# Kernel tuning notes

Measured on AMD Instinct MI355X. Metric: run time of the kernel, lower is better.

Reference implementation:

```python
import jax, jax.numpy as jnp
import numpy as np

L = 4        # num_layers
H = 1024     # hidden_size
NH = 16      # num_heads
KVH = 4      # num_kv_heads
QPK = NH // KVH
HD = H // NH # head_dim = 64
FF = 4096    # intermediate_size
V = 32000    # vocab_size
B, S = 2, 2048
EPS = 1e-5
STD = 0.02


def layernorm(x, g, b):
    m = jnp.mean(x, axis=-1, keepdims=True)
    v = jnp.mean(jnp.square(x - m), axis=-1, keepdims=True)
    return (x - m) * jax.lax.rsqrt(v + EPS) * g + b


def setup_inputs() -> dict:
    key = jax.random.key(0)
    ks = iter(jax.random.split(key, 24))
    n = lambda shape: STD * jax.random.normal(next(ks), shape, dtype=jnp.float32)
    KV = H * KVH // NH  # kv_size = 256
    inp = {
        'input_ids': jax.random.randint(next(ks), (B, S), 0, V),
        'attention_mask': jnp.zeros((B, S), dtype=jnp.float32),
        'tok_emb': n((V, H)),
        'pos_emb': n((S, H)),
        # per-layer stacked weights, stored [in, out] so y = x @ W + b
        'Wq': n((L, H, H)),  'bq': jnp.zeros((L, H)),
        'Wk': n((L, H, KV)), 'bk': jnp.zeros((L, KV)),
        'Wv': n((L, H, KV)), 'bv': jnp.zeros((L, KV)),
        'Wo': n((L, H, H)),  'bo': jnp.zeros((L, H)),
        'W1': n((L, H, FF)), 'b1': jnp.zeros((L, FF)),
        'W2': n((L, FF, H)), 'b2': jnp.zeros((L, H)),
        'ln1_g': jnp.ones((L, H)), 'ln1_b': jnp.zeros((L, H)),
        'ln2_g': jnp.ones((L, H)), 'ln2_b': jnp.zeros((L, H)),
        'lnf_g': jnp.ones((H,)),   'lnf_b': jnp.zeros((H,)),
        'Whead': n((H, V)),  # head has no bias
    }
    return inp


def gpt_forward(input_ids, attention_mask, tok_emb, pos_emb,
                Wq, bq, Wk, bk, Wv, bv, Wo, bo,
                W1, b1, W2, b2, ln1_g, ln1_b, ln2_g, ln2_b,
                lnf_g, lnf_b, Whead):
    b, s = input_ids.shape
    x = tok_emb[input_ids] + pos_emb[None, :s, :]  # [b,s,H]
    mask = attention_mask[:, None, None, None, :]  # [b,1,1,1,s] additive
    scale = 1.0 / jnp.sqrt(jnp.float32(HD))
    for l in range(L):
        h = layernorm(x, ln1_g[l], ln1_b[l])
        q = h @ Wq[l] + bq[l]                              # [b,s,H]
        k = h @ Wk[l] + bk[l]                              # [b,s,KV]
        v = h @ Wv[l] + bv[l]
        q = q.reshape(b, s, KVH, QPK, HD).transpose(0, 2, 3, 1, 4)  # [b,g,q,s,d]
        k = k.reshape(b, s, KVH, HD).transpose(0, 2, 1, 3)          # [b,g,s,d]
        v = v.reshape(b, s, KVH, HD).transpose(0, 2, 1, 3)
        scores = jnp.einsum('bgqsd,bgkd->bgqsk', q, k) * scale      # [b,g,q,s,s]
        scores = scores + mask
        w = jax.nn.softmax(scores, axis=-1)
        o = jnp.einsum('bgqsk,bgkd->bgqsd', w, v)                   # [b,g,q,s,d]
        o = o.transpose(0, 3, 1, 2, 4).reshape(b, s, H)
        x = x + (o @ Wo[l] + bo[l])
        h2 = layernorm(x, ln2_g[l], ln2_b[l])
        ff = jax.nn.gelu(h2 @ W1[l] + b1[l], approximate=False) @ W2[l] + b2[l]
        x = x + ff
    x = layernorm(x, lnf_g, lnf_b)
    return x @ Whead  # [b,s,V] logits


def reference(input_ids, attention_mask, tok_emb, pos_emb,
              Wq, bq, Wk, bk, Wv, bv, Wo, bo,
              W1, b1, W2, b2, ln1_g, ln1_b, ln2_g, ln2_b,
              lnf_g, lnf_b, Whead):
    return gpt_forward(input_ids, attention_mask, tok_emb, pos_emb,
                       Wq, bq, Wk, bk, Wv, bv, Wo, bo,
                       W1, b1, W2, b2, ln1_g, ln1_b, ln2_g, ln2_b,
                       lnf_g, lnf_b, Whead)
```

## Files before the change

### kernel.cpp

```cpp
#include <hip/hip_runtime.h>
#include <hip/hip_bf16.h>

#define LAYERS 4
#define H 1024
#define NH 16
#define KVH 4
#define HD 64
#define KVD 256
#define FF 4096
#define VOC 32000
#define BB 2
#define SS 2048
#define MROWS (BB*SS)
#define QKVN 1536

typedef __attribute__((ext_vector_type(4))) float f32x4;
typedef __attribute__((ext_vector_type(8))) short short8;
typedef __attribute__((ext_vector_type(4))) unsigned short u16x4;
typedef __attribute__((ext_vector_type(2))) unsigned int u32x2;

__device__ inline unsigned short f2bf(float f){
  union { float f; unsigned u; } v; v.f = f;
  return (unsigned short)((v.u + 0x7FFFu + ((v.u >> 16) & 1u)) >> 16);
}
__device__ inline unsigned cvt_pk_bf16(float a, float b){
  unsigned r;
  asm("v_cvt_pk_bf16_f32 %0, %1, %2" : "=v"(r) : "v"(a), "v"(b));
  return r;
}

__global__ __launch_bounds__(256) void embed_kernel(const int* __restrict__ ids,
    const float* __restrict__ tok, const float* __restrict__ pos, float* __restrict__ x)
{
  int row = blockIdx.x;
  int s = row & (SS-1);
  int id = ids[row];
  int t = threadIdx.x;
  f32x4 a = *(const f32x4*)&tok[(size_t)id*H + t*4];
  f32x4 p = *(const f32x4*)&pos[(size_t)s*H + t*4];
  *(f32x4*)&x[(size_t)row*H + t*4] = a + p;
}

__global__ __launch_bounds__(256) void ln_kernel(const float* __restrict__ x,
    const float* __restrict__ g, const float* __restrict__ b, unsigned short* __restrict__ out)
{
  int row = blockIdx.x;
  int t = threadIdx.x;
  const float* xr = x + (size_t)row*H;
  f32x4 v = *(const f32x4*)&xr[t*4];
  float s  = v[0]+v[1]+v[2]+v[3];
  float s2 = v[0]*v[0]+v[1]*v[1]+v[2]*v[2]+v[3]*v[3];
  #pragma unroll
  for (int off=1; off<64; off<<=1){ s += __shfl_xor(s,off); s2 += __shfl_xor(s2,off); }
  __shared__ float red[8];
  int w = t>>6;
  if ((t&63)==0){ red[w]=s; red[4+w]=s2; }
  __syncthreads();
  float S1 = red[0]+red[1]+red[2]+red[3];
  float S2 = red[4]+red[5]+red[6]+red[7];
  float mean = S1 * (1.0f/H);
  float var  = S2 * (1.0f/H) - mean*mean;
  float rs = rsqrtf(var + 1e-5f);
  u16x4 o;
  #pragma unroll
  for (int i=0;i<4;i++) o[i] = f2bf((v[i]-mean)*rs*g[t*4+i] + b[t*4+i]);
  *(u16x4*)&out[(size_t)row*H + t*4] = o;
}

__global__ __launch_bounds__(256) void convT_kernel(const float* __restrict__ in,
    unsigned short* __restrict__ out, int K, int N, size_t istride, size_t ostride)
{
  __shared__ float t[32][33];
  in  += (size_t)blockIdx.z * istride;
  out += (size_t)blockIdx.z * ostride;
  int n0 = blockIdx.x*32, k0 = blockIdx.y*32;
  int x = threadIdx.x & 31, y = threadIdx.x >> 5;
  #pragma unroll
  for (int j=0;j<4;j++) t[y+j*8][x] = in[(size_t)(k0+y+j*8)*N + n0 + x];
  __syncthreads();
  int x2 = threadIdx.x & 15, y2 = threadIdx.x >> 4;
  #pragma unroll
  for (int j=0;j<2;j++){
    int n = y2 + j*16;
    unsigned lo = f2bf(t[x2*2][n]);
    unsigned hi = f2bf(t[x2*2+1][n]);
    *(unsigned*)&out[(size_t)(n0+n)*K + k0 + x2*2] = lo | (hi<<16);
  }
}

__global__ __launch_bounds__(256) void bcat_kernel(const float* __restrict__ bq,
    const float* __restrict__ bk, const float* __restrict__ bv, float* __restrict__ out)
{
  int l = blockIdx.x, t = threadIdx.x;
  #pragma unroll
  for (int i=0;i<4;i++) out[l*QKVN + t + i*256] = bq[l*H + t + i*256];
  out[l*QKVN + 1024 + t] = bk[l*KVD + t];
  out[l*QKVN + 1280 + t] = bv[l*KVD + t];
}

template<int EPI>
__global__ __launch_bounds__(256) void gemm_bt(
    const unsigned short* __restrict__ A, const unsigned short* __restrict__ Bt,
    const float* __restrict__ bias, const float* __restrict__ res,
    float* __restrict__ outf, unsigned short* __restrict__ outb,
    unsigned short* __restrict__ outb2, unsigned short* __restrict__ outb3, int N, int K)
{
  __shared__ unsigned short As[128*32];
  __shared__ unsigned short Bs[128*32];
  int m0 = blockIdx.x*128, n0 = blockIdx.y*128;
  int tid = threadIdx.x;
  int lane = tid & 63, w = tid >> 6;
  int wr = (w>>1)*64, wc = (w&1)*64;
  int fr = lane & 15, fq = lane >> 4;
  f32x4 acc[4][4] = {};
  int srow = lane >> 2;
  int scol = (lane & 3) * 8;
  const unsigned short* a0 = A  + (size_t)m0*K + scol;
  const unsigned short* b0 = Bt + (size_t)n0*K + scol;
  for (int k0 = 0; k0 < K; k0 += 32){
    __syncthreads();
    #pragma unroll
    for (int c = 0; c < 2; c++){
      int ch = w*2 + c;
      int row = ch*16 + srow;
      __builtin_amdgcn_global_load_lds(
        (const __attribute__((address_space(1))) void*)(a0 + (size_t)row*K + k0),
        (__attribute__((address_space(3))) void*)(As + ch*512), 16, 0, 0);
      __builtin_amdgcn_global_load_lds(
        (const __attribute__((address_space(1))) void*)(b0 + (size_t)row*K + k0),
        (__attribute__((address_space(3))) void*)(Bs + ch*512), 16, 0, 0);
    }
    __syncthreads();
    short8 af[4], bf[4];
    #pragma unroll
    for (int mi=0;mi<4;mi++) af[mi] = *(const short8*)&As[(wr+mi*16+fr)*32 + fq*8];
    #pragma unroll
    for (int ni=0;ni<4;ni++) bf[ni] = *(const short8*)&Bs[(wc+ni*16+fr)*32 + fq*8];
    #pragma unroll
    for (int mi=0;mi<4;mi++)
      #pragma unroll
      for (int ni=0;ni<4;ni++)
        acc[mi][ni] = __builtin_amdgcn_mfma_f32_16x16x32_bf16(af[mi], bf[ni], acc[mi][ni], 0,0,0);
  }
  #pragma unroll
  for (int mi=0;mi<4;mi++)
    #pragma unroll
    for (int ni=0;ni<4;ni++){
      int col = n0 + wc + ni*16 + fr;
      float bi = (EPI==3) ? 0.0f : bias[col];
      #pragma unroll
      for (int r=0;r<4;r++){
        int row = m0 + wr + mi*16 + fq*4 + r;
        float vv = acc[mi][ni][r] + bi;
        if (EPI==1)      { size_t idx=(size_t)row*N+col; outf[idx] = vv + res[idx]; }
        else if (EPI==2) { size_t idx=(size_t)row*N+col; outb[idx] = f2bf(0.5f*vv*(1.0f+erff(vv*0.70710678118f))); }
        else if (EPI==3) { size_t idx=(size_t)row*N+col; outf[idx] = vv; }
        else if (EPI==5) {
          if (col < 1024)      outb [(size_t)row*H + col]            = f2bf(vv);
          else if (col < 1280) outb2[(size_t)row*KVD + (col-1024)]   = f2bf(vv);
          else                 outb3[(size_t)(col-1280)*MROWS + row] = f2bf(vv);
        }
      }
    }
}

template<int EPI>
__global__ __launch_bounds__(512, 2) void gemm256(
    const unsigned short* __restrict__ A, const unsigned short* __restrict__ Bt,
    const float* __restrict__ bias, float* __restrict__ outf,
    unsigned short* __restrict__ outb, int N, int K)
{
  __shared__ __align__(16) char lds[131072];
  const int tid = threadIdx.x;
  const int lane = tid & 63, wid = tid >> 6;
  const int wr = wid >> 2, wc = wid & 3;
  const int fr = lane & 15, fq = lane >> 4;
  const int m0 = blockIdx.x*256, n0 = blockIdx.y*256;
  const int nt = K >> 6;
  f32x4 acc[8][4] = {};

  #define STAGEH(PTR, baserow, kt, kk, ldsoff) do {                              \
    _Pragma("unroll")                                                            \
    for (int c=0;c<2;c++){                                                       \
      int r = c*128 + (tid>>2);                                                  \
      int ss = (tid&3) ^ ((r>>1)&3);                                             \
      __builtin_amdgcn_global_load_lds(                                          \
        (const __attribute__((address_space(1))) void*)((PTR) + (size_t)((baserow)+r)*K + (kt)*64 + (kk)*32 + ss*8), \
        (__attribute__((address_space(3))) void*)(lds + (ldsoff) + c*8192 + wid*1024), 16, 0, 0); \
    }                                                                            \
  } while(0)

  #define RD_A(buf,kk,row) (*(const short8*)(lds + ((buf)*2+(kk))*16384 + (row)*64 + ((fq ^ (((row)>>1)&3))*16)))
  #define RD_B(buf,kk,row) (*(const short8*)(lds + 65536 + ((buf)*2+(kk))*16384 + (row)*64 + ((fq ^ (((row)>>1)&3))*16)))

  STAGEH(A,  m0, 0, 0, 0);
  STAGEH(Bt, n0, 0, 0, 65536);
  STAGEH(A,  m0, 0, 1, 16384);
  STAGEH(Bt, n0, 0, 1, 65536+16384);
  asm volatile("s_waitcnt vmcnt(4)" ::: "memory");
  __builtin_amdgcn_s_barrier();

  for (int t = 0; t < nt; ++t){
    const int buf = t & 1, nb = buf ^ 1;
    const int kt1 = (t+1 < nt) ? t+1 : t;
    short8 bf[4], af[4];
    #pragma unroll
    for (int ni=0;ni<4;ni++) bf[ni] = RD_B(buf,0, wc*64+ni*16+fr);
    #pragma unroll
    for (int mi=0;mi<4;mi++) af[mi] = RD_A(buf,0, wr*128+mi*16+fr);
    STAGEH(A, m0, kt1, 0, (nb*2+0)*16384);
    __builtin_amdgcn_s_barrier();
    asm volatile("s_waitcnt lgkmcnt(0)" ::: "memory");
    __builtin_amdgcn_s_setprio(1);
    #pragma unroll
    for (int mi=0;mi<4;mi++)
      #pragma unroll
      for (int ni=0;ni<4;ni++)
        acc[mi][ni] = __builtin_amdgcn_mfma_f32_16x16x32_bf16(af[mi], bf[ni], acc[mi][ni], 0,0,0);
    __builtin_amdgcn_s_setprio(0);
    __builtin_amdgcn_s_barrier();
    #pragma unroll
    for (int mi=0;mi<4;mi++) af[mi] = RD_A(buf,0, wr*128+(4+mi)*16+fr);
    STAGEH(Bt, n0, kt1, 0, 65536+(nb*2+0)*16384);
    __builtin_amdgcn_s_barrier();
    asm volatile("s_waitcnt lgkmcnt(0)" ::: "memory");
    __builtin_amdgcn_s_setprio(1);
    #pragma unroll
    for (int mi=0;mi<4;mi++)
      #pragma unroll
      for (int ni=0;ni<4;ni++)
        acc[4+mi][ni] = __builtin_amdgcn_mfma_f32_16x16x32_bf16(af[mi], bf[ni], acc[4+mi][ni], 0,0,0);
    __builtin_amdgcn_s_setprio(0);
    asm volatile("s_waitcnt vmcnt(4)" ::: "memory");
    __builtin_amdgcn_s_barrier();
    #pragma unroll
    for (int ni=0;ni<4;ni++) bf[ni] = RD_B(buf,1, wc*64+ni*16+fr);
    #pragma unroll
    for (int mi=0;mi<4;mi++) af[mi] = RD_A(buf,1, wr*128+mi*16+fr);
    STAGEH(A, m0, kt1, 1, (nb*2+1)*16384);
    __builtin_amdgcn_s_barrier();
    asm volatile("s_waitcnt lgkmcnt(0)" ::: "memory");
    __builtin_amdgcn_s_setprio(1);
    #pragma unroll
    for (int mi=0;mi<4;mi++)
      #pragma unroll
      for (int ni=0;ni<4;ni++)
        acc[mi][ni] = __builtin_amdgcn_mfma_f32_16x16x32_bf16(af[mi], bf[ni], acc[mi][ni], 0,0,0);
    __builtin_amdgcn_s_setprio(0);
    __builtin_amdgcn_s_barrier();
    #pragma unroll
    for (int mi=0;mi<4;mi++) af[mi] = RD_A(buf,1, wr*128+(4+mi)*16+fr);
    STAGEH(Bt, n0, kt1, 1, 65536+(nb*2+1)*16384);
    __builtin_amdgcn_s_barrier();
    asm volatile("s_waitcnt lgkmcnt(0)" ::: "memory");
    __builtin_amdgcn_s_setprio(1);
    #pragma unroll
    for (int mi=0;mi<4;mi++)
      #pragma unroll
      for (int ni=0;ni<4;ni++)
        acc[4+mi][ni] = __builtin_amdgcn_mfma_f32_16x16x32_bf16(af[mi], bf[ni], acc[4+mi][ni], 0,0,0);
    __builtin_amdgcn_s_setprio(0);
    asm volatile("s_waitcnt vmcnt(4)" ::: "memory");
    __builtin_amdgcn_s_barrier();
  }
  #undef STAGEH
  #undef RD_A
  #undef RD_B

  #pragma unroll
  for (int mi=0; mi<8; mi++)
    #pragma unroll
    for (int ni=0; ni<4; ni++){
      int col = n0 + wc*64 + ni*16 + fr;
      float bi = (EPI==3) ? 0.0f : bias[col];
      #pragma unroll
      for (int r=0; r<4; r++){
        int row = m0 + wr*128 + mi*16 + fq*4 + r;
        float vv = acc[mi][ni][r] + bi;
        size_t idx = (size_t)row*N + col;
        if (EPI==3) outf[idx] = vv;
        else        outb[idx] = f2bf(0.5f*vv*(1.0f+erff(vv*0.70710678118f)));
      }
    }
}

#define LOG2E 1.4426950408889634f
__global__ __launch_bounds__(256) void attn_kernel(
    const unsigned short* __restrict__ q, const unsigned short* __restrict__ kptr,
    const unsigned short* __restrict__ vt, const float* __restrict__ mask,
    unsigned short* __restrict__ o)
{
  __shared__ char Pbuf[4][4096];
  int tid = threadIdx.x;
  int lane = tid & 63, wid = tid >> 6;
  int fr = lane & 15, fq = lane >> 4, fo = fq*8;
  int h = blockIdx.y, b = blockIdx.z, g = h >> 2;
  int qcol = h*HD, kcol = g*HD;
  int qbase = b*SS + blockIdx.x*128 + wid*32;
  char* Pl = Pbuf[wid];
  int swz = (fr & 7) << 4;

  short8 bq[2][2];
  #pragma unroll
  for (int h2=0; h2<2; h2++){
    const unsigned short* qrow = q + (size_t)(qbase + h2*16 + fr)*H + qcol;
    bq[h2][0] = *(const short8*)(qrow + fo);
    bq[h2][1] = *(const short8*)(qrow + 32 + fo);
  }

  f32x4 oacc[2][4] = {};
  float mrun[2] = {-1e30f, -1e30f}, lsum[2] = {0.f, 0.f};
  const float sc2 = 0.125f * LOG2E;

  const unsigned short* kp[4];
  #pragma unroll
  for (int f=0; f<4; f++) kp[f] = kptr + (size_t)(b*SS + f*16 + fr)*KVD + kcol + fo;
  const unsigned short* vp[4];
  #pragma unroll
  for (int dc=0; dc<4; dc++) vp[dc] = vt + (size_t)(kcol + dc*16 + fr)*MROWS + b*SS + fo;
  const float* mp = mask + b*SS + fq*4;

  short8 kaA[4][2], kaB[4][2];
  #pragma unroll
  for (int f=0; f<4; f++){
    kaA[f][0] = *(const short8*)(kp[f]);
    kaA[f][1] = *(const short8*)(kp[f] + 32);
    kp[f] += 64*KVD;
  }

#define ATTN_STEP(KA, KB, PF) do {                                             \
    f32x4 mkv[4];                                                              \
    _Pragma("unroll")                                                          \
    for (int f=0; f<4; f++) mkv[f] = *(const f32x4*)(mp + f*16);               \
    short8 va[4][2];                                                           \
    _Pragma("unroll")                                                          \
    for (int dc=0; dc<4; dc++){                                                \
      va[dc][0] = *(const short8*)(vp[dc]);                                    \
      va[dc][1] = *(const short8*)(vp[dc] + 32);                               \
    }                                                                          \
    f32x4 sf[2][4] = {};                                                       \
    __builtin_amdgcn_s_setprio(1);                                             \
    _Pragma("unroll")                                                          \
    for (int h2=0; h2<2; h2++)                                                 \
      _Pragma("unroll")                                                        \
      for (int f=0; f<4; f++){                                                 \
        sf[h2][f] = __builtin_amdgcn_mfma_f32_16x16x32_bf16(KA[f][0], bq[h2][0], sf[h2][f],0,0,0); \
        sf[h2][f] = __builtin_amdgcn_mfma_f32_16x16x32_bf16(KA[f][1], bq[h2][1], sf[h2][f],0,0,0); \
      }                                                                        \
    __builtin_amdgcn_s_setprio(0);                                             \
    if (PF){                                                                   \
      _Pragma("unroll")                                                        \
      for (int f=0; f<4; f++){                                                 \
        KB[f][0] = *(const short8*)(kp[f]);                                    \
        KB[f][1] = *(const short8*)(kp[f] + 32);                               \
        kp[f] += 64*KVD;                                                       \
      }                                                                        \
    }                                                                          \
    _Pragma("unroll")                                                          \
    for (int f=0; f<4; f++){                                                   \
      _Pragma("unroll")                                                        \
      for (int r=0; r<4; r++){                                                 \
        float m2 = mkv[f][r]*LOG2E;                                            \
        sf[0][f][r] = sf[0][f][r]*sc2 + m2;                                    \
        sf[1][f][r] = sf[1][f][r]*sc2 + m2;                                    \
      }                                                                        \
    }                                                                          \
    float pm[2];                                                               \
    _Pragma("unroll")                                                          \
    for (int h2=0; h2<2; h2++){                                                \
      float a0 = fmaxf(fmaxf(sf[h2][0][0],sf[h2][0][1]), fmaxf(sf[h2][0][2],sf[h2][0][3])); \
      float a1 = fmaxf(fmaxf(sf[h2][1][0],sf[h2][1][1]), fmaxf(sf[h2][1][2],sf[h2][1][3])); \
      float a2 = fmaxf(fmaxf(sf[h2][2][0],sf[h2][2][1]), fmaxf(sf[h2][2][2],sf[h2][2][3])); \
      float a3 = fmaxf(fmaxf(sf[h2][3][0],sf[h2][3][1]), fmaxf(sf[h2][3][2],sf[h2][3][3])); \
      float p = fmaxf(fmaxf(a0,a1), fmaxf(a2,a3));                             \
      p = fmaxf(p, __shfl_xor(p, 16));                                         \
      p = fmaxf(p, __shfl_xor(p, 32));                                         \
      pm[h2] = p;                                                              \
    }                                                                          \
    if (!__all(pm[0] <= mrun[0]+8.f && pm[1] <= mrun[1]+8.f)){                 \
      float al[2];                                                             \
      _Pragma("unroll")                                                        \
      for (int h2=0; h2<2; h2++){                                              \
        float mn = fmaxf(mrun[h2], pm[h2]);                                    \
        al[h2] = __builtin_amdgcn_exp2f(mrun[h2]-mn);                          \
        mrun[h2] = mn;                                                         \
        lsum[h2] *= al[h2];                                                    \
      }                                                                        \
      _Pragma("unroll")                                                        \
      for (int r=0; r<4; r++){                                                 \
        float altl = __shfl(al[0], fq*4+r);                                    \
        float alth = __shfl(al[1], fq*4+r);                                    \
        _Pragma("unroll")                                                      \
        for (int dc=0; dc<4; dc++){ oacc[0][dc][r]*=altl; oacc[1][dc][r]*=alth; } \
      }                                                                        \
    }                                                                          \
    _Pragma("unroll")                                                          \
    for (int h2=0; h2<2; h2++){                                                \
      float ps = 0.f;                                                          \
      _Pragma("unroll")                                                        \
      for (int f=0; f<4; f++)                                                  \
        _Pragma("unroll")                                                      \
        for (int r=0; r<4; r++){                                               \
          float e = __builtin_amdgcn_exp2f(sf[h2][f][r]-mrun[h2]);             \
          sf[h2][f][r] = e; ps += e;                                           \
        }                                                                      \
      ps += __shfl_xor(ps, 16);                                                \
      ps += __shfl_xor(ps, 32);                                                \
      lsum[h2] += ps;                                                          \
    }                                                                          \
    _Pragma("unroll")                                                          \
    for (int h2=0; h2<2; h2++){                                                \
      int prow = h2*16 + fr;                                                   \
      _Pragma("unroll")                                                        \
      for (int f=0; f<4; f++){                                                 \
        u32x2 pw;                                                              \
        pw[0] = cvt_pk_bf16(sf[h2][f][0], sf[h2][f][1]);                       \
        pw[1] = cvt_pk_bf16(sf[h2][f][2], sf[h2][f][3]);                       \
        *(u32x2*)(Pl + prow*128 + ((f*32 + fq*8) ^ swz)) = pw;                 \
      }                                                                        \
    }                                                                          \
    __builtin_amdgcn_s_setprio(1);                                             \
    _Pragma("unroll")                                                          \
    for (int h2=0; h2<2; h2++){                                                \
      int prow = h2*16 + fr;                                                   \
      _Pragma("unroll")                                                        \
      for (int gs=0; gs<2; gs++){                                              \
        short8 pa = *(const short8*)(Pl + prow*128 + ((gs*64 + fq*16) ^ swz)); \
        _Pragma("unroll")                                                      \
        for (int dc=0; dc<4; dc++)                                             \
          oacc[h2][dc] = __builtin_amdgcn_mfma_f32_16x16x32_bf16(pa, va[dc][gs], oacc[h2][dc],0,0,0); \
      }                                                                        \
    }                                                                          \
    __builtin_amdgcn_s_setprio(0);                                             \
    _Pragma("unroll")                                                          \
    for (int dc=0; dc<4; dc++) vp[dc] += 64;                                   \
    mp += 64;                                                                  \
  } while(0)

  for (int it = 0; it < SS/128 - 1; ++it){
    ATTN_STEP(kaA, kaB, 1);
    ATTN_STEP(kaB, kaA, 1);
  }
  ATTN_STEP(kaA, kaB, 1);
  ATTN_STEP(kaB, kaA, 0);
#undef ATTN_STEP

  #pragma unroll
  for (int h2=0; h2<2; h2++){
    float lt[4];
    #pragma unroll
    for (int r=0; r<4; r++) lt[r] = __shfl(lsum[h2], fq*4+r);
    #pragma unroll
    for (int dc=0; dc<4; dc++)
      #pragma unroll
      for (int r=0; r<4; r++){
        int row = qbase + h2*16 + fq*4 + r;
        o[(size_t)row*H + qcol + dc*16 + fr] = f2bf(oacc[h2][dc][r] / lt[r]);
      }
  }
}

extern "C" void kernel_launch(void* const* d_in, const int* in_sizes, int n_in,
                              void* d_out, int out_size, void* d_ws, size_t ws_size,
                              hipStream_t stream)
{
  const int*   ids  = (const int*)  d_in[0];
  const float* mask = (const float*)d_in[1];
  const float* tok  = (const float*)d_in[2];
  const float* pos  = (const float*)d_in[3];
  const float* Wq   = (const float*)d_in[4];
  const float* bq   = (const float*)d_in[5];
  const float* Wk   = (const float*)d_in[6];
  const float* bk   = (const float*)d_in[7];
  const float* Wv   = (const float*)d_in[8];
  const float* bv   = (const float*)d_in[9];
  const float* Wo   = (const float*)d_in[10];
  const float* bo   = (const float*)d_in[11];
  const float* W1   = (const float*)d_in[12];
  const float* b1   = (const float*)d_in[13];
  const float* W2   = (const float*)d_in[14];
  const float* b2   = (const float*)d_in[15];
  const float* ln1g = (const float*)d_in[16];
  const float* ln1b = (const float*)d_in[17];
  const float* ln2g = (const float*)d_in[18];
  const float* ln2b = (const float*)d_in[19];
  const float* lnfg = (const float*)d_in[20];
  const float* lnfb = (const float*)d_in[21];
  const float* Wh   = (const float*)d_in[22];
  float* out = (float*)d_out;

  char* ws = (char*)d_ws;
  float*          x    = (float*)ws;          ws += (size_t)MROWS*H*4;
  unsigned short* hb   = (unsigned short*)ws; ws += (size_t)MROWS*H*2;
  unsigned short* qb   = (unsigned short*)ws; ws += (size_t)MROWS*H*2;
  unsigned short* kb   = (unsigned short*)ws; ws += (size_t)MROWS*KVD*2;
  unsigned short* vtb  = (unsigned short*)ws; ws += (size_t)KVD*MROWS*2;
  unsigned short* ob   = (unsigned short*)ws; ws += (size_t)MROWS*H*2;
  unsigned short* f1   = (unsigned short*)ws; ws += (size_t)MROWS*FF*2;
  unsigned short* Wqkv = (unsigned short*)ws; ws += (size_t)LAYERS*QKVN*H*2;
  unsigned short* WoT  = (unsigned short*)ws; ws += (size_t)LAYERS*H*H*2;
  unsigned short* W1T  = (unsigned short*)ws; ws += (size_t)LAYERS*H*FF*2;
  unsigned short* W2T  = (unsigned short*)ws; ws += (size_t)LAYERS*H*FF*2;
  unsigned short* WhT  = (unsigned short*)ws; ws += (size_t)H*VOC*2;
  float*          bcat = (float*)ws;          ws += (size_t)LAYERS*QKVN*4;

  convT_kernel<<<dim3(H/32,   H/32,  LAYERS), 256, 0, stream>>>(Wq, Wqkv,          H,  H,   (size_t)H*H,   (size_t)QKVN*H);
  convT_kernel<<<dim3(KVD/32, H/32,  LAYERS), 256, 0, stream>>>(Wk, Wqkv + 1024*H, H,  KVD, (size_t)H*KVD, (size_t)QKVN*H);
  convT_kernel<<<dim3(KVD/32, H/32,  LAYERS), 256, 0, stream>>>(Wv, Wqkv + 1280*H, H,  KVD, (size_t)H*KVD, (size_t)QKVN*H);
  convT_kernel<<<dim3(H/32,   H/32,  LAYERS), 256, 0, stream>>>(Wo, WoT,           H,  H,   (size_t)H*H,   (size_t)H*H);
  convT_kernel<<<dim3(FF/32,  H/32,  LAYERS), 256, 0, stream>>>(W1, W1T,           H,  FF,  (size_t)H*FF,  (size_t)H*FF);
  convT_kernel<<<dim3(H/32,   FF/32, LAYERS), 256, 0, stream>>>(W2, W2T,           FF, H,   (size_t)FF*H,  (size_t)FF*H);
  convT_kernel<<<dim3(VOC/32, H/32,  1),      256, 0, stream>>>(Wh, WhT,           H,  VOC, 0, 0);
  bcat_kernel<<<LAYERS, 256, 0, stream>>>(bq, bk, bv, bcat);

  embed_kernel<<<MROWS, 256, 0, stream>>>(ids, tok, pos, x);
  for (int l=0; l<LAYERS; l++){
    ln_kernel<<<MROWS,256,0,stream>>>(x, ln1g + l*H, ln1b + l*H, hb);
    gemm_bt<5><<<dim3(MROWS/128, QKVN/128),256,0,stream>>>(hb, Wqkv + (size_t)l*QKVN*H, bcat + l*QKVN, nullptr, nullptr, qb, kb, vtb, QKVN, H);
    attn_kernel<<<dim3(SS/128, NH, BB), 256, 0, stream>>>(qb, kb, vtb, mask, ob);
    gemm_bt<1><<<dim3(MROWS/128, H/128),  256,0,stream>>>(ob, WoT + (size_t)l*H*H,  bo + l*H,  x, x, nullptr, nullptr, nullptr, H, H);
    ln_kernel<<<MROWS,256,0,stream>>>(x, ln2g + l*H, ln2b + l*H, hb);
    gemm256<2><<<dim3(MROWS/256, FF/256), 512,0,stream>>>(hb, W1T + (size_t)l*H*FF, b1 + l*FF, nullptr, f1, FF, H);
    gemm_bt<1><<<dim3(MROWS/128, H/128),  256,0,stream>>>(f1, W2T + (size_t)l*H*FF, b2 + l*H,  x, x, nullptr, nullptr, nullptr, H, FF);
  }
  ln_kernel<<<MROWS,256,0,stream>>>(x, lnfg, lnfb, hb);
  gemm256<3><<<dim3(MROWS/256, VOC/256), 512,0,stream>>>(hb, WhT, nullptr, out, nullptr, VOC, H);
}
```

Measured before the change: 1.989 ms.

## Deepen GEMM pipelines to 4-stage LDS ring and remap workgroups across XCDs

The small 128x128 GEMM moves from a single-buffered, fully synchronised loop to a 4-stage global_load_lds ring with swizzled LDS, prefetching three k-tiles ahead and waiting with vmcnt, so loads overlap MFMA work. The 256x256 GEMM switches from a 2-buffer scheme with 64-wide k-tiles to a 4-buffer ring with 32-wide k-tiles. It also remaps block IDs so each XCD gets a contiguous range of tiles, which should improve L2 reuse. The cost is more LDS per block in gemm_bt, which may limit occupancy, plus added launch-bounds pressure on registers.

Result: faster. 1.688 ms (-15.2%).

```diff
diff --git a/kernel.cpp b/kernel.cpp
--- a/kernel.cpp
+++ b/kernel.cpp
@@ -99,49 +99,67 @@
 }
 
 template<int EPI>
-__global__ __launch_bounds__(256) void gemm_bt(
+__global__ __launch_bounds__(256, 2) void gemm_bt(
     const unsigned short* __restrict__ A, const unsigned short* __restrict__ Bt,
     const float* __restrict__ bias, const float* __restrict__ res,
     float* __restrict__ outf, unsigned short* __restrict__ outb,
     unsigned short* __restrict__ outb2, unsigned short* __restrict__ outb3, int N, int K)
 {
-  __shared__ unsigned short As[128*32];
-  __shared__ unsigned short Bs[128*32];
-  int m0 = blockIdx.x*128, n0 = blockIdx.y*128;
-  int tid = threadIdx.x;
-  int lane = tid & 63, w = tid >> 6;
-  int wr = (w>>1)*64, wc = (w&1)*64;
-  int fr = lane & 15, fq = lane >> 4;
+  __shared__ __align__(16) char lds[65536];
+  const int tid = threadIdx.x;
+  const int lane = tid & 63, wid = tid >> 6;
+  const int wr = (wid>>1)*64, wc = (wid&1)*64;
+  const int fr = lane & 15, fq = lane >> 4;
+  const int m0 = blockIdx.x*128, n0 = blockIdx.y*128;
+  const int nt = K >> 5;
   f32x4 acc[4][4] = {};
-  int srow = lane >> 2;
-  int scol = (lane & 3) * 8;
-  const unsigned short* a0 = A  + (size_t)m0*K + scol;
-  const unsigned short* b0 = Bt + (size_t)n0*K + scol;
-  for (int k0 = 0; k0 < K; k0 += 32){
-    __syncthreads();
-    #pragma unroll
-    for (int c = 0; c < 2; c++){
-      int ch = w*2 + c;
-      int row = ch*16 + srow;
-      __builtin_amdgcn_global_load_lds(
-        (const __attribute__((address_space(1))) void*)(a0 + (size_t)row*K + k0),
-        (__attribute__((address_space(3))) void*)(As + ch*512), 16, 0, 0);
-      __builtin_amdgcn_global_load_lds(
-        (const __attribute__((address_space(1))) void*)(b0 + (size_t)row*K + k0),
-        (__attribute__((address_space(3))) void*)(Bs + ch*512), 16, 0, 0);
-    }
-    __syncthreads();
+
+  #define STG1(PTR, baserow, kt, ldsoff) do {                                   \
+    _Pragma("unroll")                                                           \
+    for (int c=0;c<2;c++){                                                      \
+      int rr = c*64 + (tid>>2);                                                 \
+      int ss = (tid&3) ^ ((rr>>1)&3);                                           \
+      __builtin_amdgcn_global_load_lds(                                         \
+        (const __attribute__((address_space(1))) void*)((PTR) + (size_t)((baserow)+rr)*K + (kt)*32 + ss*8), \
+        (__attribute__((address_space(3))) void*)(lds + (ldsoff) + c*4096 + wid*1024), 16, 0, 0); \
+    }                                                                           \
+  } while(0)
+  #define RDA1(buf,row) (*(const short8*)(lds + (buf)*16384 + (row)*64 + ((fq ^ (((row)>>1)&3))*16)))
+  #define RDB1(buf,row) (*(const short8*)(lds + (buf)*16384 + 8192 + (row)*64 + ((fq ^ (((row)>>1)&3))*16)))
+
+  STG1(A,  m0, 0, 0);      STG1(Bt, n0, 0, 8192);
+  STG1(A,  m0, 1, 16384);  STG1(Bt, n0, 1, 16384+8192);
+  STG1(A,  m0, 2, 32768);  STG1(Bt, n0, 2, 32768+8192);
+  asm volatile("s_waitcnt vmcnt(8)" ::: "memory");
+  __builtin_amdgcn_s_barrier();
+
+  for (int t = 0; t < nt; ++t){
+    const int buf = t & 3;
+    const int s3 = (t+3) & 3;
+    const int t3 = (t+3 < nt) ? t+3 : t;
     short8 af[4], bf[4];
     #pragma unroll
-    for (int mi=0;mi<4;mi++) af[mi] = *(const short8*)&As[(wr+mi*16+fr)*32 + fq*8];
-    #pragma unroll
-    for (int ni=0;ni<4;ni++) bf[ni] = *(const short8*)&Bs[(wc+ni*16+fr)*32 + fq*8];
+    for (int mi=0;mi<4;mi++) af[mi] = RDA1(buf, wr+mi*16+fr);
+    #pragma unroll
+    for (int ni=0;ni<4;ni++) bf[ni] = RDB1(buf, wc+ni*16+fr);
+    STG1(A,  m0, t3, s3*16384);
+    STG1(Bt, n0, t3, s3*16384+8192);
+    __builtin_amdgcn_s_barrier();
+    asm volatile("s_waitcnt lgkmcnt(0)" ::: "memory");
+    __builtin_amdgcn_s_setprio(1);
     #pragma unroll
     for (int mi=0;mi<4;mi++)
       #pragma unroll
       for (int ni=0;ni<4;ni++)
         acc[mi][ni] = __builtin_amdgcn_mfma_f32_16x16x32_bf16(af[mi], bf[ni], acc[mi][ni], 0,0,0);
-  }
+    __builtin_amdgcn_s_setprio(0);
+    asm volatile("s_waitcnt vmcnt(8)" ::: "memory");
+    __builtin_amdgcn_s_barrier();
+  }
+  #undef STG1
+  #undef RDA1
+  #undef RDB1
+
   #pragma unroll
   for (int mi=0;mi<4;mi++)
     #pragma unroll
@@ -173,42 +191,46 @@
   __shared__ __align__(16) char lds[131072];
   const int tid = threadIdx.x;
   const int lane = tid & 63, wid = tid >> 6;
-  const int wr = wid >> 2, wc = wid & 3;
+  const int wr = wid >> 3, wc = wid & 3;
+  const int wrr = wid >> 2;
   const int fr = lane & 15, fq = lane >> 4;
-  const int m0 = blockIdx.x*256, n0 = blockIdx.y*256;
-  const int nt = K >> 6;
+  const int nwg = gridDim.x * gridDim.y;
+  const int orig = blockIdx.x + blockIdx.y * gridDim.x;
+  const int q = nwg >> 3, r = nwg & 7, xcd = orig & 7, off = orig >> 3;
+  const int wg = (xcd < r ? xcd*(q+1) : r*(q+1) + (xcd - r)*q) + off;
+  const int m0 = (wg % gridDim.x) * 256, n0 = (wg / gridDim.x) * 256;
+  const int nt = K >> 5;
   f32x4 acc[8][4] = {};
 
-  #define STAGEH(PTR, baserow, kt, kk, ldsoff) do {                              \
-    _Pragma("unroll")                                                            \
-    for (int c=0;c<2;c++){                                                       \
-      int r = c*128 + (tid>>2);                                                  \
-      int ss = (tid&3) ^ ((r>>1)&3);                                             \
-      __builtin_amdgcn_global_load_lds(                                          \
-        (const __attribute__((address_space(1))) void*)((PTR) + (size_t)((baserow)+r)*K + (kt)*64 + (kk)*32 + ss*8), \
+  #define STG(PTR, baserow, kt, ldsoff) do {                                    \
+    _Pragma("unroll")                                                           \
+    for (int c=0;c<2;c++){                                                      \
+      int rr = c*128 + (tid>>2);                                                \
+      int ss = (tid&3) ^ ((rr>>1)&3);                                           \
+      __builtin_amdgcn_global_load_lds(                                         \
+        (const __attribute__((address_space(1))) void*)((PTR) + (size_t)((baserow)+rr)*K + (kt)*32 + ss*8), \
         (__attribute__((address_space(3))) void*)(lds + (ldsoff) + c*8192 + wid*1024), 16, 0, 0); \
-    }                                                                            \
+    }                                                                           \
   } while(0)
-
-  #define RD_A(buf,kk,row) (*(const short8*)(lds + ((buf)*2+(kk))*16384 + (row)*64 + ((fq ^ (((row)>>1)&3))*16)))
-  #define RD_B(buf,kk,row) (*(const short8*)(lds + 65536 + ((buf)*2+(kk))*16384 + (row)*64 + ((fq ^ (((row)>>1)&3))*16)))
-
-  STAGEH(A,  m0, 0, 0, 0);
-  STAGEH(Bt, n0, 0, 0, 65536);
-  STAGEH(A,  m0, 0, 1, 16384);
-  STAGEH(Bt, n0, 0, 1, 65536+16384);
-  asm volatile("s_waitcnt vmcnt(4)" ::: "memory");
+  #define RDA(buf,row) (*(const short8*)(lds + (buf)*32768 + (row)*64 + ((fq ^ (((row)>>1)&3))*16)))
+  #define RDB(buf,row) (*(const short8*)(lds + (buf)*32768 + 16384 + (row)*64 + ((fq ^ (((row)>>1)&3))*16)))
+
+  STG(A,  m0, 0, 0);      STG(Bt, n0, 0, 16384);
+  STG(A,  m0, 1, 32768);  STG(Bt, n0, 1, 32768+16384);
+  STG(A,  m0, 2, 65536);  STG(Bt, n0, 2, 65536+16384);
+  asm volatile("s_waitcnt vmcnt(8)" ::: "memory");
   __builtin_amdgcn_s_barrier();
 
   for (int t = 0; t < nt; ++t){
-    const int buf = t & 1, nb = buf ^ 1;
-    const int kt1 = (t+1 < nt) ? t+1 : t;
+    const int buf = t & 3;
+    const int s3 = (t+3) & 3;
+    const int t3 = (t+3 < nt) ? t+3 : t;
     short8 bf[4], af[4];
     #pragma unroll
-    for (int ni=0;ni<4;ni++) bf[ni] = RD_B(buf,0, wc*64+ni*16+fr);
-    #pragma unroll
-    for (int mi=0;mi<4;mi++) af[mi] = RD_A(buf,0, wr*128+mi*16+fr);
-    STAGEH(A, m0, kt1, 0, (nb*2+0)*16384);
+    for (int ni=0;ni<4;ni++) bf[ni] = RDB(buf, wc*64+ni*16+fr);
+    #pragma unroll
+    for (int mi=0;mi<4;mi++) af[mi] = RDA(buf, wrr*128+mi*16+fr);
+    STG(A, m0, t3, s3*32768);
     __builtin_amdgcn_s_barrier();
     asm volatile("s_waitcnt lgkmcnt(0)" ::: "memory");
     __builtin_amdgcn_s_setprio(1);
@@ -220,8 +242,8 @@
     __builtin_amdgcn_s_setprio(0);
     __builtin_amdgcn_s_barrier();
     #pragma unroll
-    for (int mi=0;mi<4;mi++) af[mi] = RD_A(buf,0, wr*128+(4+mi)*16+fr);
-    STAGEH(Bt, n0, kt1, 0, 65536+(nb*2+0)*16384);
+    for (int mi=0;mi<4;mi++) af[mi] = RDA(buf, wrr*128+(4+mi)*16+fr);
+    STG(Bt, n0, t3, s3*32768+16384);
     __builtin_amdgcn_s_barrier();
     asm volatile("s_waitcnt lgkmcnt(0)" ::: "memory");
     __builtin_amdgcn_s_setprio(1);
@@ -231,41 +253,12 @@
       for (int ni=0;ni<4;ni++)
         acc[4+mi][ni] = __builtin_amdgcn_mfma_f32_16x16x32_bf16(af[mi], bf[ni], acc[4+mi][ni], 0,0,0);
     __builtin_amdgcn_s_setprio(0);
-    asm volatile("s_waitcnt vmcnt(4)" ::: "memory");
+    asm volatile("s_waitcnt vmcnt(8)" ::: "memory");
     __builtin_amdgcn_s_barrier();
-    #pragma unroll
-    for (int ni=0;ni<4;ni++) bf[ni] = RD_B(buf,1, wc*64+ni*16+fr);
-    #pragma unroll
-    for (int mi=0;mi<4;mi++) af[mi] = RD_A(buf,1, wr*128+mi*16+fr);
-    STAGEH(A, m0, kt1, 1, (nb*2+1)*16384);
-    __builtin_amdgcn_s_barrier();
-    asm volatile("s_waitcnt lgkmcnt(0)" ::: "memory");
-    __builtin_amdgcn_s_setprio(1);
-    #pragma unroll
-    for (int mi=0;mi<4;mi++)
-      #pragma unroll
-      for (int ni=0;ni<4;ni++)
-        acc[mi][ni] = __builtin_amdgcn_mfma_f32_16x16x32_bf16(af[mi], bf[ni], acc[mi][ni], 0,0,0);
-    __builtin_amdgcn_s_setprio(0);
-    __builtin_amdgcn_s_barrier();
-    #pragma unroll
-    for (int mi=0;mi<4;mi++) af[mi] = RD_A(buf,1, wr*128+(4+mi)*16+fr);
-    STAGEH(Bt, n0, kt1, 1, 65536+(nb*2+1)*16384);
-    __builtin_amdgcn_s_barrier();
-    asm volatile("s_waitcnt lgkmcnt(0)" ::: "memory");
-    __builtin_amdgcn_s_setprio(1);
-    #pragma unroll
-    for (int mi=0;mi<4;mi++)
-      #pragma unroll
-      for (int ni=0;ni<4;ni++)
-        acc[4+mi][ni] = __builtin_amdgcn_mfma_f32_16x16x32_bf16(af[mi], bf[ni], acc[4+mi][ni], 0,0,0);
-    __builtin_amdgcn_s_setprio(0);
-    asm volatile("s_waitcnt vmcnt(4)" ::: "memory");
-    __builtin_amdgcn_s_barrier();
-  }
-  #undef STAGEH
-  #undef RD_A
-  #undef RD_B
+  }
+  #undef STG
+  #undef RDA
+  #undef RDB
 
   #pragma unroll
   for (int mi=0; mi<8; mi++)
@@ -275,7 +268,7 @@
       float bi = (EPI==3) ? 0.0f : bias[col];
       #pragma unroll
       for (int r=0; r<4; r++){
-        int row = m0 + wr*128 + mi*16 + fq*4 + r;
+        int row = m0 + wrr*128 + mi*16 + fq*4 + r;
         float vv = acc[mi][ni][r] + bi;
         size_t idx = (size_t)row*N + col;
         if (EPI==3) outf[idx] = vv;
```
